# Performance work log

Hardware: AMD Instinct MI355X
Metric: run time of the kernel (lower is better)

Reference implementation:

```python
import jax, jax.numpy as jnp
import numpy as np
from jax import lax

B, T, D, H = 256, 1024, 64, 64


def setup_inputs() -> dict:
    key = jax.random.key(0)
    ks = jax.random.split(key, 16)
    def n(k, shape, s=0.1):
        return (jax.random.normal(k, shape) * s).astype(jnp.float32)
    return {
        "x": jax.random.normal(ks[0], (B, T, D), dtype=jnp.float32),
        "mask": (jax.random.uniform(ks[1], (B, T, D)) < 0.8).astype(jnp.float32),
        # params stacked over direction axis [2, ...]: 0=fwd RITS, 1=bwd RITS
        "Wih": n(ks[2], (2, 4 * H, 2 * D)),   # LSTMCell weight_ih
        "Whh": n(ks[3], (2, 4 * H, H)),       # LSTMCell weight_hh
        "bih": n(ks[4], (2, 4 * H)),
        "bhh": n(ks[5], (2, 4 * H)),
        "Wdh": n(ks[6], (2, H, D)),           # TemporalDecay h (dense)
        "bdh": n(ks[7], (2, H)),
        "wdx": n(ks[8], (2, D)),              # TemporalDecay x (diag -> vector)
        "bdx": n(ks[9], (2, D)),
        "Whr": n(ks[10], (2, D, H)),          # hist_reg
        "bhr": n(ks[11], (2, D)),
        "Wfr": n(ks[12], (2, D, D)),          # feat_reg (zero-diag applied in fwd)
        "bfr": n(ks[13], (2, D)),
        "Wwc": n(ks[14], (2, D, 2 * D)),      # weight_combine
        "bwc": n(ks[15], (2, D)),
    }


def _run_rits(x, m, Wih, Whh, bih, bhh, Wdh, bdh, wdx, bdx, Whr, bhr, Wfr, bfr, Wwc, bwc):
    # x, m: [B, T, D]
    Bs, Ts, Ds = x.shape
    Hs = Whh.shape[-1]
    xT = jnp.swapaxes(x, 0, 1)  # [T, B, D]
    mT = jnp.swapaxes(m, 0, 1)

    # delta[0]=0; delta[t] = 1 + (1-m[t-1]) * delta[t-1]
    def dstep(carry, m_t):
        return 1.0 + (1.0 - m_t) * carry, carry
    _, delta = lax.scan(dstep, jnp.zeros((Bs, Ds), x.dtype), mT)  # [T, B, D]

    eye = jnp.eye(Ds, dtype=x.dtype)
    WfrM = Wfr * (1.0 - eye)

    def step(carry, inp):
        h, c = carry
        x_s, m_s, d = inp
        gamma_h = jnp.exp(-jax.nn.relu(d @ Wdh.T + bdh))              # [B, H]
        x_h = h @ Whr.T + bhr
        x_c = m_s * x_s + (1.0 - m_s) * x_h
        h = h * gamma_h
        z_h = x_c @ WfrM.T + bfr
        gamma_x = jnp.exp(-jax.nn.relu(d * wdx + bdx))                 # diag temporal decay
        alpha = jax.nn.sigmoid(jnp.concatenate([gamma_x, m_s], -1) @ Wwc.T + bwc)
        c_h = alpha * z_h + (1.0 - alpha) * x_h
        c_c = m_s * x_s + (1.0 - m_s) * c_h
        gates = jnp.concatenate([c_c, m_s], -1) @ Wih.T + bih + h @ Whh.T + bhh
        i, f, g, o = jnp.split(gates, 4, axis=-1)
        c_n = jax.nn.sigmoid(f) * c + jax.nn.sigmoid(i) * jnp.tanh(g)
        h_n = jax.nn.sigmoid(o) * jnp.tanh(c_n)
        return (h_n, c_n), (c_c, c_h, z_h, x_h)

    h0 = jnp.zeros((Bs, Hs), x.dtype)
    _, outs = lax.scan(step, (h0, h0), (xT, mT, delta))
    return tuple(jnp.swapaxes(o, 0, 1) for o in outs)  # each [B, T, D]


def reference(x, mask, Wih, Whh, bih, bhh, Wdh, bdh, wdx, bdx, Whr, bhr, Wfr, bfr, Wwc, bwc):
    xs = jnp.stack([x, x[:, ::-1, :]])          # [2, B, T, D]
    ms = jnp.stack([mask, mask[:, ::-1, :]])
    cc, ch, zh, xh = jax.vmap(_run_rits)(xs, ms, Wih, Whh, bih, bhh, Wdh, bdh,
                                         wdx, bdx, Whr, bhr, Wfr, bfr, Wwc, bwc)

    def both(a):  # [2,B,T,D] -> [B,2,T,D], bwd direction re-reversed in time
        return jnp.stack([a[0], a[1][:, ::-1, :]], axis=1)

    imputation = both(cc)                              # [B, 2, T, D]
    out = jnp.mean(imputation, axis=1)[..., None]      # [B, T, D, 1]
    predictions = jnp.concatenate([both(ch), both(zh), both(xh)], axis=1)[..., None]  # [B,6,T,D,1]
    predictions = jnp.swapaxes(predictions, 0, 1)      # [6, B, T, D, 1]
    return out, predictions
```

## Files before the change

kernel.cpp:

```cpp
#include <hip/hip_runtime.h>


constexpr int NB = 256;
constexpr int NT = 1024;
constexpr int ND = 64;
constexpr int NG = 256;
constexpr int K2 = 128;

__device__ __forceinline__ float sgm(float v){ return 1.0f/(1.0f+__expf(-v)); }
__device__ __forceinline__ float tnh(float v){
  float a = fabsf(v);
  float e = __expf(-2.0f*a);
  float t = (1.0f-e)/(1.0f+e);
  return v < 0.0f ? -t : t;
}

__device__ __forceinline__ float dot64r(const float* __restrict__ wr,
                                        const float* __restrict__ act){
  float a0=0.f,a1=0.f,a2=0.f,a3=0.f;
  #pragma unroll
  for (int k=0;k<64;k+=4){
    const float4 v = *(const float4*)(act+k);
    a0 = fmaf(wr[k+0], v.x, a0);
    a1 = fmaf(wr[k+1], v.y, a1);
    a2 = fmaf(wr[k+2], v.z, a2);
    a3 = fmaf(wr[k+3], v.w, a3);
  }
  return (a0+a1)+(a2+a3);
}

__device__ __forceinline__ float dot32r(const float* __restrict__ wr,
                                        const float* __restrict__ act){
  float a0=0.f,a1=0.f,a2=0.f,a3=0.f;
  #pragma unroll
  for (int k=0;k<32;k+=4){
    const float4 v = *(const float4*)(act+k);
    a0 = fmaf(wr[k+0], v.x, a0);
    a1 = fmaf(wr[k+1], v.y, a1);
    a2 = fmaf(wr[k+2], v.z, a2);
    a3 = fmaf(wr[k+3], v.w, a3);
  }
  return (a0+a1)+(a2+a3);
}

__global__ __launch_bounds__(512, 1) void brits_fused(
    const float* __restrict__ x_g, const float* __restrict__ m_g,
    const float* __restrict__ Wih_g, const float* __restrict__ Whh_g,
    const float* __restrict__ bih_g, const float* __restrict__ bhh_g,
    const float* __restrict__ Wdh_g, const float* __restrict__ bdh_g,
    const float* __restrict__ wdx_g, const float* __restrict__ bdx_g,
    const float* __restrict__ Whr_g, const float* __restrict__ bhr_g,
    const float* __restrict__ Wfr_g, const float* __restrict__ bfr_g,
    const float* __restrict__ Wwc_g, const float* __restrict__ bwc_g,
    float* __restrict__ out0, float* __restrict__ pred)
{
  const int tid = threadIdx.x;
  const int w   = tid >> 6;
  const int l   = tid & 63;
  const int bid = blockIdx.x;
  const int dir = bid >> 7;
  const int pair = bid & 127;
  const int b0 = pair*2, b1 = pair*2+1;

  const float* Wih_d = Wih_g + (size_t)dir*NG*K2;
  const float* Whh_d = Whh_g + (size_t)dir*NG*ND;
  const float* bih_d = bih_g + dir*NG;
  const float* bhh_d = bhh_g + dir*NG;
  const float* Wdh_d = Wdh_g + dir*ND*ND;
  const float* bdh_d = bdh_g + dir*ND;
  const float* wdx_d = wdx_g + dir*ND;
  const float* bdx_d = bdx_g + dir*ND;
  const float* Whr_d = Whr_g + dir*ND*ND;
  const float* bhr_d = bhr_g + dir*ND;
  const float* Wfr_d = Wfr_g + dir*ND*ND;
  const float* bfr_d = bfr_g + dir*ND;
  const float* Wwc_d = Wwc_g + dir*ND*K2;
  const float* bwc_d = bwc_g + dir*ND;

  __shared__ __align__(16) float h_s [2][ND];
  __shared__ __align__(16) float hd_s[2][ND];
  __shared__ __align__(16) float xh_s[2][ND];
  __shared__ __align__(16) float xc_s[2][ND];
  __shared__ __align__(16) float zp_s[2][2][ND];
  __shared__ __align__(16) float al_s[2][ND];
  __shared__ __align__(16) float gh_s[2][ND];
  __shared__ __align__(16) float gx_s[2][ND];
  __shared__ __align__(16) float dl_s[2][ND];
  __shared__ __align__(16) float cc_s[2][ND];
  __shared__ __align__(16) float gt_s[2][NG];
  __shared__ __align__(16) float xb_s[2][2][ND];
  __shared__ __align__(16) float mb_s[2][2][ND];

  float wa[K2];
  float wb[ND];
  float bias0 = 0.f;
  float wdx_l = 0.f, bdx_l = 0.f, bfr_l = 0.f;

  if (w == 1){
    #pragma unroll
    for (int k=0;k<ND;k+=4){
      const float4 v = *(const float4*)(Whr_d + l*ND + k);
      wa[k]=v.x; wa[k+1]=v.y; wa[k+2]=v.z; wa[k+3]=v.w;
    }
    bias0 = bhr_d[l];
  } else if (w == 2){
    #pragma unroll
    for (int k=0;k<K2;k+=4){
      const float4 v = *(const float4*)(Wwc_d + l*K2 + k);
      wa[k]=v.x; wa[k+1]=v.y; wa[k+2]=v.z; wa[k+3]=v.w;
    }
    #pragma unroll
    for (int k=0;k<32;k+=4){
      const float4 v = *(const float4*)(Wfr_d + l*ND + k);
      wb[k]   = (k==l)   ? 0.f : v.x;
      wb[k+1] = (k+1==l) ? 0.f : v.y;
      wb[k+2] = (k+2==l) ? 0.f : v.z;
      wb[k+3] = (k+3==l) ? 0.f : v.w;
    }
    bias0 = bwc_d[l];
  } else if (w == 3){
    #pragma unroll
    for (int k=0;k<ND;k+=4){
      const float4 v = *(const float4*)(Wdh_d + l*ND + k);
      wa[k]=v.x; wa[k+1]=v.y; wa[k+2]=v.z; wa[k+3]=v.w;
    }
    #pragma unroll
    for (int k=0;k<32;k+=4){
      const float4 v = *(const float4*)(Wfr_d + l*ND + 32 + k);
      wb[k]   = (32+k==l)   ? 0.f : v.x;
      wb[k+1] = (32+k+1==l) ? 0.f : v.y;
      wb[k+2] = (32+k+2==l) ? 0.f : v.z;
      wb[k+3] = (32+k+3==l) ? 0.f : v.w;
    }
    bias0 = bdh_d[l];
  } else if (w >= 4){
    const int r = (w-4)*64 + l;
    #pragma unroll
    for (int k=0;k<K2;k+=4){
      const float4 v = *(const float4*)(Wih_d + r*K2 + k);
      wa[k]=v.x; wa[k+1]=v.y; wa[k+2]=v.z; wa[k+3]=v.w;
    }
    #pragma unroll
    for (int k=0;k<ND;k+=4){
      const float4 v = *(const float4*)(Whh_d + r*ND + k);
      wb[k]=v.x; wb[k+1]=v.y; wb[k+2]=v.z; wb[k+3]=v.w;
    }
    bias0 = bih_d[r] + bhh_d[r];
  }
  if (w < 2){
    wdx_l = wdx_d[l]; bdx_l = bdx_d[l]; bfr_l = bfr_d[l];
  }

  float cst = 0.f;
  float dlt = 0.f;

  if (w == 0){
    #pragma unroll
    for (int s=0;s<2;++s){ h_s[s][l]=0.f; hd_s[s][l]=0.f; dl_s[s][l]=0.f; }
    const int t0 = dir ? (NT-1) : 0;
    #pragma unroll
    for (int s=0;s<2;++s){
      const int bbs = s ? b1 : b0;
      xb_s[0][s][l] = x_g[((size_t)bbs*NT + t0)*ND + l];
      mb_s[0][s][l] = m_g[((size_t)bbs*NT + t0)*ND + l];
    }
  }
  if (w < 2){
    gx_s[w][l] = __expf(-fmaxf(0.f, bdx_l));
  }
  __syncthreads();
  if (w == 2){
    #pragma unroll
    for (int s=0;s<2;++s){
      const float acc = bias0 + dot64r(wa, &gx_s[s][0]) + dot64r(wa+64, &mb_s[0][s][0]);
      al_s[s][l] = sgm(acc);
    }
  }
  __syncthreads();

  for (int t=0; t<NT; ++t){
    const int cur = t & 1;
    const int nxt = cur ^ 1;
    const int tm  = dir ? (NT-1-t) : t;

    float ghh0 = 0.f, ghh1 = 0.f;
    if (w == 0){
      if (t+1 < NT){
        const int tn = dir ? (NT-2-t) : (t+1);
        #pragma unroll
        for (int s=0;s<2;++s){
          const int bbs = s ? b1 : b0;
          xb_s[nxt][s][l] = x_g[((size_t)bbs*NT + tn)*ND + l];
          mb_s[nxt][s][l] = m_g[((size_t)bbs*NT + tn)*ND + l];
        }
      }
    } else if (w == 1){
      #pragma unroll
      for (int s=0;s<2;++s){
        const float xh = bias0 + dot64r(wa, &h_s[s][0]);
        xh_s[s][l] = xh;
        const float mm = mb_s[cur][s][l];
        const float xx = xb_s[cur][s][l];
        xc_s[s][l] = mm*xx + (1.f-mm)*xh;
        const int bbs = s ? b1 : b0;
        pred[(size_t)(4+dir)*NB*NT*ND + ((size_t)bbs*NT + tm)*ND + l] = xh;
      }
    } else if (w >= 4){
      ghh0 = bias0 + dot64r(wb, &hd_s[0][0]);
      ghh1 = bias0 + dot64r(wb, &hd_s[1][0]);
    }
    __syncthreads();
    if (w == 2){
      zp_s[0][0][l] = dot32r(wb, &xc_s[0][0]);
      zp_s[0][1][l] = dot32r(wb, &xc_s[1][0]);
    } else if (w == 3){
      zp_s[1][0][l] = dot32r(wb, &xc_s[0][32]);
      zp_s[1][1][l] = dot32r(wb, &xc_s[1][32]);
    }
    __syncthreads();
    if (w < 2){
      const int s = w;
      const int bbs = s ? b1 : b0;
      const float mm = mb_s[cur][s][l];
      const float xx = xb_s[cur][s][l];
      const float zh = zp_s[0][s][l] + zp_s[1][s][l] + bfr_l;
      const float a  = al_s[s][l];
      const float xh = xh_s[s][l];
      const float ch = a*zh + (1.f-a)*xh;
      const float cc = mm*xx + (1.f-mm)*ch;
      cc_s[s][l] = cc;
      const size_t ob = ((size_t)bbs*NT + tm)*ND + l;
      pred[(size_t)(0+dir)*NB*NT*ND + ob] = ch;
      pred[(size_t)(2+dir)*NB*NT*ND + ob] = zh;
      atomicAdd(&out0[ob], 0.5f*cc);
      dlt = 1.0f + (1.0f-mm)*dlt;
      dl_s[s][l] = dlt;
      gx_s[s][l] = __expf(-fmaxf(0.f, fmaf(dlt, wdx_l, bdx_l)));
    }
    __syncthreads();
    if (w >= 4){
      const float g0 = ghh0 + dot64r(wa, &cc_s[0][0]) + dot64r(wa+64, &mb_s[cur][0][0]);
      const float g1 = ghh1 + dot64r(wa, &cc_s[1][0]) + dot64r(wa+64, &mb_s[cur][1][0]);
      const int r = (w-4)*64 + l;
      gt_s[0][r] = g0;
      gt_s[1][r] = g1;
    } else if (w == 2){
      if (t+1 < NT){
        #pragma unroll
        for (int s=0;s<2;++s){
          const float acc = bias0 + dot64r(wa, &gx_s[s][0]) + dot64r(wa+64, &mb_s[nxt][s][0]);
          al_s[s][l] = sgm(acc);
        }
      }
    } else if (w == 3){
      if (t+1 < NT){
        #pragma unroll
        for (int s=0;s<2;++s){
          gh_s[s][l] = __expf(-fmaxf(0.f, bias0 + dot64r(wa, &dl_s[s][0])));
        }
      }
    }
    __syncthreads();
    if (w < 2){
      const int s = w;
      const float gi = gt_s[s][l];
      const float gf = gt_s[s][64+l];
      const float gg = gt_s[s][128+l];
      const float go = gt_s[s][192+l];
      cst = sgm(gf)*cst + sgm(gi)*tnh(gg);
      const float hn = sgm(go)*tnh(cst);
      h_s[s][l]  = hn;
      hd_s[s][l] = hn * gh_s[s][l];
    }
    __syncthreads();
  }
}

extern "C" void kernel_launch(void* const* d_in, const int* in_sizes, int n_in,
                              void* d_out, int out_size, void* d_ws, size_t ws_size,
                              hipStream_t stream) {
  (void)in_sizes; (void)n_in; (void)d_ws; (void)ws_size; (void)out_size;
  const float* x   = (const float*)d_in[0];
  const float* m   = (const float*)d_in[1];
  const float* Wih = (const float*)d_in[2];
  const float* Whh = (const float*)d_in[3];
  const float* bih = (const float*)d_in[4];
  const float* bhh = (const float*)d_in[5];
  const float* Wdh = (const float*)d_in[6];
  const float* bdh = (const float*)d_in[7];
  const float* wdx = (const float*)d_in[8];
  const float* bdx = (const float*)d_in[9];
  const float* Whr = (const float*)d_in[10];
  const float* bhr = (const float*)d_in[11];
  const float* Wfr = (const float*)d_in[12];
  const float* bfr = (const float*)d_in[13];
  const float* Wwc = (const float*)d_in[14];
  const float* bwc = (const float*)d_in[15];

  float* out  = (float*)d_out;
  float* pred = out + (size_t)NB*NT*ND;

  hipMemsetAsync(out, 0, (size_t)NB*NT*ND*sizeof(float), stream);

  brits_fused<<<dim3(256), dim3(512), 0, stream>>>(
      x, m, Wih, Whh, bih, bhh, Wdh, bdh, wdx, bdx,
      Whr, bhr, Wfr, bfr, Wwc, bwc, out, pred);
}
```

Before: 13.19 ms.

## Split LSTM gate dots across all waves and move small weights to swizzled LDS

Restructures the per-timestep schedule. The LSTM gate matvec now runs on all 8 waves, each lane covering half a row, with the halves combined by a cross-lane shuffle. The small regression and decay weights (Whr, Wfr, Wdh, Wwc) move from registers into XOR-swizzled shared memory. The history and feature regressions are merged into one wave phase per sample, which cuts the loop from five barriers to three, and the barriers become a raw lgkmcnt wait plus s_barrier. This is meant to shorten the serial critical path of each timestep and lower register pressure (launch bounds now allow 2 blocks per CU). In exchange, the regression dots become serial inside waves 0/1 and read weights from LDS instead of registers.

```diff
diff --git a/kernel.cpp b/kernel.cpp
--- a/kernel.cpp
+++ b/kernel.cpp
@@ -15,35 +15,59 @@
   return v < 0.0f ? -t : t;
 }
 
-__device__ __forceinline__ float dot64r(const float* __restrict__ wr,
-                                        const float* __restrict__ act){
+__device__ __forceinline__ void bar(){
+  asm volatile("s_waitcnt lgkmcnt(0)" ::: "memory");
+  __builtin_amdgcn_s_barrier();
+}
+
+__device__ __forceinline__ float dot64_sw(const float* wrow, int swl,
+                                          const float* act){
   float a0=0.f,a1=0.f,a2=0.f,a3=0.f;
   #pragma unroll
-  for (int k=0;k<64;k+=4){
-    const float4 v = *(const float4*)(act+k);
-    a0 = fmaf(wr[k+0], v.x, a0);
-    a1 = fmaf(wr[k+1], v.y, a1);
-    a2 = fmaf(wr[k+2], v.z, a2);
-    a3 = fmaf(wr[k+3], v.w, a3);
+  for (int k4=0;k4<16;++k4){
+    const float4 wv = *(const float4*)(wrow + ((k4^swl)<<2));
+    const float4 av = *(const float4*)(act + (k4<<2));
+    a0=fmaf(wv.x,av.x,a0); a1=fmaf(wv.y,av.y,a1);
+    a2=fmaf(wv.z,av.z,a2); a3=fmaf(wv.w,av.w,a3);
   }
   return (a0+a1)+(a2+a3);
 }
 
-__device__ __forceinline__ float dot32r(const float* __restrict__ wr,
-                                        const float* __restrict__ act){
+__device__ __forceinline__ float dot128_sw(const float* wrow, int swl,
+                                           const float* actA, const float* actB){
   float a0=0.f,a1=0.f,a2=0.f,a3=0.f;
   #pragma unroll
-  for (int k=0;k<32;k+=4){
-    const float4 v = *(const float4*)(act+k);
-    a0 = fmaf(wr[k+0], v.x, a0);
-    a1 = fmaf(wr[k+1], v.y, a1);
-    a2 = fmaf(wr[k+2], v.z, a2);
-    a3 = fmaf(wr[k+3], v.w, a3);
+  for (int k4=0;k4<32;++k4){
+    const float4 wv = *(const float4*)(wrow + ((k4^swl)<<2));
+    const float4 av = (k4<16) ? *(const float4*)(actA + (k4<<2))
+                              : *(const float4*)(actB + (((k4-16))<<2));
+    a0=fmaf(wv.x,av.x,a0); a1=fmaf(wv.y,av.y,a1);
+    a2=fmaf(wv.z,av.z,a2); a3=fmaf(wv.w,av.w,a3);
   }
   return (a0+a1)+(a2+a3);
 }
 
-__global__ __launch_bounds__(512, 1) void brits_fused(
+#define GATE_DOT(res, ACT) do{                                           \
+    float a0=0.f,a1=0.f,a2=0.f,a3=0.f;                                   \
+    _Pragma("unroll")                                                    \
+    for (int k=0;k<64;k+=4){                                             \
+      const float4 av = *(const float4*)((ACT)+k);                       \
+      a0=fmaf(wg_ih[k  ],av.x,a0); a1=fmaf(wg_ih[k+1],av.y,a1);          \
+      a2=fmaf(wg_ih[k+2],av.z,a2); a3=fmaf(wg_ih[k+3],av.w,a3);          \
+    }                                                                    \
+    res = (a0+a1)+(a2+a3); }while(0)
+
+#define PHH_DOT(res, ACT) do{                                            \
+    float a0=0.f,a1=0.f,a2=0.f,a3=0.f;                                   \
+    _Pragma("unroll")                                                    \
+    for (int k=0;k<32;k+=4){                                             \
+      const float4 av = *(const float4*)((ACT)+k);                       \
+      a0=fmaf(wg_hh[k  ],av.x,a0); a1=fmaf(wg_hh[k+1],av.y,a1);          \
+      a2=fmaf(wg_hh[k+2],av.z,a2); a3=fmaf(wg_hh[k+3],av.w,a3);          \
+    }                                                                    \
+    res = (a0+a1)+(a2+a3); }while(0)
+
+__global__ __launch_bounds__(512, 2) void brits_fused(
     const float* __restrict__ x_g, const float* __restrict__ m_g,
     const float* __restrict__ Wih_g, const float* __restrict__ Whh_g,
     const float* __restrict__ bih_g, const float* __restrict__ bhh_g,
@@ -55,8 +79,11 @@
     float* __restrict__ out0, float* __restrict__ pred)
 {
   const int tid = threadIdx.x;
-  const int w   = tid >> 6;
   const int l   = tid & 63;
+  const int w   = __builtin_amdgcn_readfirstlane(tid >> 6);
+  const int h   = l >> 5;
+  const int r   = w*32 + (l & 31);
+  const int swl = l & 7;
   const int bid = blockIdx.x;
   const int dir = bid >> 7;
   const int pair = bid & 127;
@@ -77,190 +104,167 @@
   const float* Wwc_d = Wwc_g + dir*ND*K2;
   const float* bwc_d = bwc_g + dir*ND;
 
+  __shared__ __align__(16) float Whr_sw[64*64];
+  __shared__ __align__(16) float Wfr_sw[64*64];
+  __shared__ __align__(16) float Wdh_sw[64*64];
+  __shared__ __align__(16) float Wwc_sw[64*128];
   __shared__ __align__(16) float h_s [2][ND];
   __shared__ __align__(16) float hd_s[2][ND];
-  __shared__ __align__(16) float xh_s[2][ND];
   __shared__ __align__(16) float xc_s[2][ND];
-  __shared__ __align__(16) float zp_s[2][2][ND];
+  __shared__ __align__(16) float cc_s[2][ND];
+  __shared__ __align__(16) float dl_s[2][ND];
+  __shared__ __align__(16) float gx_s[2][ND];
+  __shared__ __align__(16) float gh_s[2][ND];
   __shared__ __align__(16) float al_s[2][ND];
-  __shared__ __align__(16) float gh_s[2][ND];
-  __shared__ __align__(16) float gx_s[2][ND];
-  __shared__ __align__(16) float dl_s[2][ND];
-  __shared__ __align__(16) float cc_s[2][ND];
   __shared__ __align__(16) float gt_s[2][NG];
   __shared__ __align__(16) float xb_s[2][2][ND];
   __shared__ __align__(16) float mb_s[2][2][ND];
 
-  float wa[K2];
-  float wb[ND];
-  float bias0 = 0.f;
-  float wdx_l = 0.f, bdx_l = 0.f, bfr_l = 0.f;
-
-  if (w == 1){
+  {
     #pragma unroll
-    for (int k=0;k<ND;k+=4){
-      const float4 v = *(const float4*)(Whr_d + l*ND + k);
-      wa[k]=v.x; wa[k+1]=v.y; wa[k+2]=v.z; wa[k+3]=v.w;
-    }
-    bias0 = bhr_d[l];
-  } else if (w == 2){
+    for (int q=0;q<2;++q){
+      const int k4 = 2*w + q;
+      float4 v;
+      v = *(const float4*)(Whr_d + l*ND + 4*k4);
+      *(float4*)(Whr_sw + l*64 + ((k4^swl)<<2)) = v;
+      v = *(const float4*)(Wdh_d + l*ND + 4*k4);
+      *(float4*)(Wdh_sw + l*64 + ((k4^swl)<<2)) = v;
+      v = *(const float4*)(Wfr_d + l*ND + 4*k4);
+      const int c = 4*k4;
+      if (c   == l) v.x = 0.f;
+      if (c+1 == l) v.y = 0.f;
+      if (c+2 == l) v.z = 0.f;
+      if (c+3 == l) v.w = 0.f;
+      *(float4*)(Wfr_sw + l*64 + ((k4^swl)<<2)) = v;
+    }
     #pragma unroll
-    for (int k=0;k<K2;k+=4){
-      const float4 v = *(const float4*)(Wwc_d + l*K2 + k);
-      wa[k]=v.x; wa[k+1]=v.y; wa[k+2]=v.z; wa[k+3]=v.w;
-    }
-    #pragma unroll
-    for (int k=0;k<32;k+=4){
-      const float4 v = *(const float4*)(Wfr_d + l*ND + k);
-      wb[k]   = (k==l)   ? 0.f : v.x;
-      wb[k+1] = (k+1==l) ? 0.f : v.y;
-      wb[k+2] = (k+2==l) ? 0.f : v.z;
-      wb[k+3] = (k+3==l) ? 0.f : v.w;
-    }
-    bias0 = bwc_d[l];
-  } else if (w == 3){
-    #pragma unroll
-    for (int k=0;k<ND;k+=4){
-      const float4 v = *(const float4*)(Wdh_d + l*ND + k);
-      wa[k]=v.x; wa[k+1]=v.y; wa[k+2]=v.z; wa[k+3]=v.w;
-    }
-    #pragma unroll
-    for (int k=0;k<32;k+=4){
-      const float4 v = *(const float4*)(Wfr_d + l*ND + 32 + k);
-      wb[k]   = (32+k==l)   ? 0.f : v.x;
-      wb[k+1] = (32+k+1==l) ? 0.f : v.y;
-      wb[k+2] = (32+k+2==l) ? 0.f : v.z;
-      wb[k+3] = (32+k+3==l) ? 0.f : v.w;
-    }
-    bias0 = bdh_d[l];
-  } else if (w >= 4){
-    const int r = (w-4)*64 + l;
-    #pragma unroll
-    for (int k=0;k<K2;k+=4){
-      const float4 v = *(const float4*)(Wih_d + r*K2 + k);
-      wa[k]=v.x; wa[k+1]=v.y; wa[k+2]=v.z; wa[k+3]=v.w;
-    }
-    #pragma unroll
-    for (int k=0;k<ND;k+=4){
-      const float4 v = *(const float4*)(Whh_d + r*ND + k);
-      wb[k]=v.x; wb[k+1]=v.y; wb[k+2]=v.z; wb[k+3]=v.w;
-    }
-    bias0 = bih_d[r] + bhh_d[r];
-  }
-  if (w < 2){
-    wdx_l = wdx_d[l]; bdx_l = bdx_d[l]; bfr_l = bfr_d[l];
-  }
+    for (int q=0;q<4;++q){
+      const int k4 = 4*w + q;
+      float4 v = *(const float4*)(Wwc_d + l*K2 + 4*k4);
+      *(float4*)(Wwc_sw + l*128 + ((k4^swl)<<2)) = v;
+    }
+  }
+
+  float wg_ih[64];
+  float wg_hh[32];
+  #pragma unroll
+  for (int k=0;k<64;k+=4){
+    const float4 v = *(const float4*)(Wih_d + (size_t)r*K2 + h*64 + k);
+    wg_ih[k]=v.x; wg_ih[k+1]=v.y; wg_ih[k+2]=v.z; wg_ih[k+3]=v.w;
+  }
+  #pragma unroll
+  for (int k=0;k<32;k+=4){
+    const float4 v = *(const float4*)(Whh_d + (size_t)r*ND + h*32 + k);
+    wg_hh[k]=v.x; wg_hh[k+1]=v.y; wg_hh[k+2]=v.z; wg_hh[k+3]=v.w;
+  }
+  const float gbias = bih_d[r] + bhh_d[r];
+
+  float bhr_l=0.f, bfr_l=0.f, wdx_l=0.f, bdx_l=0.f, bdh_l=0.f, bwc_l=0.f;
+  const float* whr_row = Whr_sw + l*64;
+  const float* wfr_row = Wfr_sw + l*64;
+  const float* wdh_row = Wdh_sw + l*64;
+  const float* wwc_row = Wwc_sw + l*128;
+  if (w < 2){ bhr_l = bhr_d[l]; bfr_l = bfr_d[l]; wdx_l = wdx_d[l]; bdx_l = bdx_d[l]; }
+  if (w==4 || w==5){ bdh_l = bdh_d[l]; }
+  if (w>=6){ bwc_l = bwc_d[l]; }
 
   float cst = 0.f;
   float dlt = 0.f;
+  float xr  = 0.f, mr = 0.f;
+
+  const size_t NBTD  = (size_t)NB*NT*ND;
+  const size_t plane0 = (size_t)(0+dir)*NBTD;
+  const size_t plane2 = (size_t)(2+dir)*NBTD;
+  const size_t plane4 = (size_t)(4+dir)*NBTD;
 
   if (w == 0){
-    #pragma unroll
-    for (int s=0;s<2;++s){ h_s[s][l]=0.f; hd_s[s][l]=0.f; dl_s[s][l]=0.f; }
+    h_s[0][l]=0.f; h_s[1][l]=0.f; hd_s[0][l]=0.f; hd_s[1][l]=0.f;
+  }
+  if (w==2 || w==3){
+    const int s = w-2;
+    const int bbs = s ? b1 : b0;
     const int t0 = dir ? (NT-1) : 0;
-    #pragma unroll
-    for (int s=0;s<2;++s){
-      const int bbs = s ? b1 : b0;
-      xb_s[0][s][l] = x_g[((size_t)bbs*NT + t0)*ND + l];
-      mb_s[0][s][l] = m_g[((size_t)bbs*NT + t0)*ND + l];
-    }
+    const size_t ib = ((size_t)bbs*NT + t0)*ND + l;
+    xb_s[0][s][l] = x_g[ib];
+    mb_s[0][s][l] = m_g[ib];
   }
   if (w < 2){
     gx_s[w][l] = __expf(-fmaxf(0.f, bdx_l));
   }
-  __syncthreads();
-  if (w == 2){
-    #pragma unroll
-    for (int s=0;s<2;++s){
-      const float acc = bias0 + dot64r(wa, &gx_s[s][0]) + dot64r(wa+64, &mb_s[0][s][0]);
-      al_s[s][l] = sgm(acc);
-    }
-  }
-  __syncthreads();
+  bar();
+  if (w >= 6){
+    const int s = w-6;
+    al_s[s][l] = sgm(bwc_l + dot128_sw(wwc_row, swl, &gx_s[s][0], &mb_s[0][s][0]));
+  }
+  bar();
 
   for (int t=0; t<NT; ++t){
     const int cur = t & 1;
     const int nxt = cur ^ 1;
     const int tm  = dir ? (NT-1-t) : t;
 
-    float ghh0 = 0.f, ghh1 = 0.f;
-    if (w == 0){
-      if (t+1 < NT){
-        const int tn = dir ? (NT-2-t) : (t+1);
-        #pragma unroll
-        for (int s=0;s<2;++s){
-          const int bbs = s ? b1 : b0;
-          xb_s[nxt][s][l] = x_g[((size_t)bbs*NT + tn)*ND + l];
-          mb_s[nxt][s][l] = m_g[((size_t)bbs*NT + tn)*ND + l];
-        }
-      }
-    } else if (w == 1){
-      #pragma unroll
-      for (int s=0;s<2;++s){
-        const float xh = bias0 + dot64r(wa, &h_s[s][0]);
-        xh_s[s][l] = xh;
-        const float mm = mb_s[cur][s][l];
-        const float xx = xb_s[cur][s][l];
-        xc_s[s][l] = mm*xx + (1.f-mm)*xh;
-        const int bbs = s ? b1 : b0;
-        pred[(size_t)(4+dir)*NB*NT*ND + ((size_t)bbs*NT + tm)*ND + l] = xh;
-      }
-    } else if (w >= 4){
-      ghh0 = bias0 + dot64r(wb, &hd_s[0][0]);
-      ghh1 = bias0 + dot64r(wb, &hd_s[1][0]);
-    }
-    __syncthreads();
-    if (w == 2){
-      zp_s[0][0][l] = dot32r(wb, &xc_s[0][0]);
-      zp_s[0][1][l] = dot32r(wb, &xc_s[1][0]);
-    } else if (w == 3){
-      zp_s[1][0][l] = dot32r(wb, &xc_s[0][32]);
-      zp_s[1][1][l] = dot32r(wb, &xc_s[1][32]);
-    }
-    __syncthreads();
+    float phh0, phh1;
+    PHH_DOT(phh0, &hd_s[0][h*32]);
+    PHH_DOT(phh1, &hd_s[1][h*32]);
+
     if (w < 2){
       const int s = w;
       const int bbs = s ? b1 : b0;
+      const size_t ob = ((size_t)bbs*NT + tm)*ND + l;
+      const float xh = bhr_l + dot64_sw(whr_row, swl, &h_s[s][0]);
+      pred[plane4 + ob] = xh;
       const float mm = mb_s[cur][s][l];
       const float xx = xb_s[cur][s][l];
-      const float zh = zp_s[0][s][l] + zp_s[1][s][l] + bfr_l;
+      const float xc = mm*xx + (1.f-mm)*xh;
+      xc_s[s][l] = xc;
+      dlt = 1.0f + (1.0f-mm)*dlt;
+      dl_s[s][l] = dlt;
+      gx_s[s][l] = __expf(-fmaxf(0.f, fmaf(dlt, wdx_l, bdx_l)));
+      const float zh = bfr_l + dot64_sw(wfr_row, swl, &xc_s[s][0]);
+      pred[plane2 + ob] = zh;
       const float a  = al_s[s][l];
-      const float xh = xh_s[s][l];
       const float ch = a*zh + (1.f-a)*xh;
       const float cc = mm*xx + (1.f-mm)*ch;
       cc_s[s][l] = cc;
-      const size_t ob = ((size_t)bbs*NT + tm)*ND + l;
-      pred[(size_t)(0+dir)*NB*NT*ND + ob] = ch;
-      pred[(size_t)(2+dir)*NB*NT*ND + ob] = zh;
+      pred[plane0 + ob] = ch;
       atomicAdd(&out0[ob], 0.5f*cc);
-      dlt = 1.0f + (1.0f-mm)*dlt;
-      dl_s[s][l] = dlt;
-      gx_s[s][l] = __expf(-fmaxf(0.f, fmaf(dlt, wdx_l, bdx_l)));
-    }
-    __syncthreads();
-    if (w >= 4){
-      const float g0 = ghh0 + dot64r(wa, &cc_s[0][0]) + dot64r(wa+64, &mb_s[cur][0][0]);
-      const float g1 = ghh1 + dot64r(wa, &cc_s[1][0]) + dot64r(wa+64, &mb_s[cur][1][0]);
-      const int r = (w-4)*64 + l;
-      gt_s[0][r] = g0;
-      gt_s[1][r] = g1;
-    } else if (w == 2){
+    } else if (w < 4){
       if (t+1 < NT){
-        #pragma unroll
-        for (int s=0;s<2;++s){
-          const float acc = bias0 + dot64r(wa, &gx_s[s][0]) + dot64r(wa+64, &mb_s[nxt][s][0]);
-          al_s[s][l] = sgm(acc);
-        }
+        const int s = w-2;
+        const int bbs = s ? b1 : b0;
+        const int tn = dir ? (NT-2-t) : (t+1);
+        const size_t ib = ((size_t)bbs*NT + tn)*ND + l;
+        xr = x_g[ib];
+        mr = m_g[ib];
       }
-    } else if (w == 3){
+    }
+    bar();
+
+    {
+      float g0, g1;
+      GATE_DOT(g0, h ? &mb_s[cur][0][0] : &cc_s[0][0]);
+      GATE_DOT(g1, h ? &mb_s[cur][1][0] : &cc_s[1][0]);
+      g0 += phh0;
+      g1 += phh1;
+      g0 += __shfl_xor(g0, 32, 64);
+      g1 += __shfl_xor(g1, 32, 64);
+      if (h == 0){
+        gt_s[0][r] = g0 + gbias;
+        gt_s[1][r] = g1 + gbias;
+      }
+    }
+    if (w==2 || w==3){
       if (t+1 < NT){
-        #pragma unroll
-        for (int s=0;s<2;++s){
-          gh_s[s][l] = __expf(-fmaxf(0.f, bias0 + dot64r(wa, &dl_s[s][0])));
-        }
+        const int s = w-2;
+        xb_s[nxt][s][l] = xr;
+        mb_s[nxt][s][l] = mr;
       }
-    }
-    __syncthreads();
+    } else if ((w==4 || w==5) && (t+1 < NT)){
+      const int s = w-4;
+      gh_s[s][l] = __expf(-fmaxf(0.f, bdh_l + dot64_sw(wdh_row, swl, &dl_s[s][0])));
+    }
+    bar();
+
     if (w < 2){
       const int s = w;
       const float gi = gt_s[s][l];
@@ -271,8 +275,11 @@
       const float hn = sgm(go)*tnh(cst);
       h_s[s][l]  = hn;
       hd_s[s][l] = hn * gh_s[s][l];
-    }
-    __syncthreads();
+    } else if (w >= 6 && (t+1 < NT)){
+      const int s = w-6;
+      al_s[s][l] = sgm(bwc_l + dot128_sw(wwc_row, swl, &gx_s[s][0], &mb_s[nxt][s][0]));
+    }
+    bar();
   }
 }
 
```

Result: faster. 12.77 ms (-3.2%).
